# Optimization experiments

Measured on AMD Instinct MI355X. Metric: run time of the kernel, lower is better.

## Reference

```python
import jax, jax.numpy as jnp
import numpy as np

IM_H, IM_W = 240, 320
ENV_R, ENV_C = 120, 160
ENV_H, ENV_W = 8, 16
GRID = 8
NGRIDS = 6 * GRID * GRID  # 384


def _normalize(v, axis, eps=1e-6):
    return v / (jnp.linalg.norm(v, axis=axis, keepdims=True) + eps)


def setup_inputs() -> dict:
    key = jax.random.key(0)
    k1, k2, k3, k4 = jax.random.split(key, 4)
    B = 2
    normalPred = jax.random.normal(k1, (B, 3, IM_H, IM_W), dtype=jnp.float32)
    # positive depth in [0.5, 5.0] so z = -depth passes the z < -0.1 mask mostly
    depthPred = jax.random.uniform(k2, (B, IM_H, IM_W), dtype=jnp.float32, minval=0.5, maxval=5.0)
    envmapsPredImage = jax.random.uniform(k3, (B, 3, ENV_R, ENV_C, ENV_H, ENV_W), dtype=jnp.float32)
    # intrinsics must have cx = W/2, cy = H/2 (module asserts f_W_scale == f_H_scale)
    cam_K = jnp.tile(jnp.array([[300.0, 0.0, IM_W / 2.0],
                                [0.0, 300.0, IM_H / 2.0],
                                [0.0, 0.0, 1.0]], dtype=jnp.float32)[None], (B, 1, 1))
    # grid-cell centers of the 6 layout faces in LightNet coords (normally from get_grid_centers)
    verts_center_lightNet = jax.random.normal(k4, (B, 6, GRID, GRID, 3), dtype=jnp.float32) * 3.0
    return {"normalPred": normalPred, "depthPred": depthPred,
            "envmapsPredImage": envmapsPredImage, "cam_K": cam_K,
            "verts_center_lightNet": verts_center_lightNet}


def _forward(normalPred, depthPred, envmapsPredImage, cam_K, verts_center_lightNet):
    B = depthPred.shape[0]
    dt = depthPred.dtype
    # ---- back-project per-pixel 3D points from depth + intrinsics ----
    u0, v0 = IM_W / 2.0, IM_H / 2.0
    vv, uu = jnp.meshgrid(jnp.arange(IM_H, dtype=dt), jnp.arange(IM_W, dtype=dt), indexing='ij')
    f_pix = (cam_K[:, 0, 0] * (IM_W / 2.0) / cam_K[:, 0, 2]).reshape(B, 1, 1)
    z = -depthPred
    x = -(uu - u0) / f_pix * z
    y = (vv - v0) / f_pix * z
    points = jnp.stack([x, y, z], axis=1)  # [B,3,IM_H,IM_W]

    # ---- renderingLayer.forwardEnv (if_normal_only): per-pixel local frame at env res ----
    r = IM_H // ENV_R  # = IM_W // ENV_C = 2
    n = normalPred.reshape(B, 3, ENV_R, r, ENV_C, r).mean(axis=(3, 5))
    normal = _normalize(n, axis=1)                              # [B,3,eR,eC]
    up = jnp.array([0.0, 1.0, 0.0], dtype=dt).reshape(1, 3, 1, 1)
    camyProj = (up * normal).sum(axis=1, keepdims=True) * normal
    camy = _normalize(up - camyProj, axis=1)
    camx = -_normalize(jnp.cross(camy, normal, axis=1), axis=1)

    # ---- accu_light ----
    pts_s = points[:, :, ::r, ::r].transpose(0, 2, 3, 1)        # [B,eR,eC,3]
    mask = pts_s[..., 2] < -0.1                                 # [B,eR,eC]
    p_t = verts_center_lightNet.reshape(B, NGRIDS, 1, 1, 3)
    vec_to_t = p_t - pts_s[:, None]                             # [B,G,eR,eC,3]

    # A columns = [camx, camy, normal]; invert per pixel
    A = jnp.stack([camx.transpose(0, 2, 3, 1),
                   camy.transpose(0, 2, 3, 1),
                   normal.transpose(0, 2, 3, 1)], axis=-1)      # [B,eR,eC,3,3]
    A = A + 1e-6 * jnp.eye(3, dtype=dt)
    invA = jnp.linalg.inv(A)

    l_local = jnp.einsum('bhwij,bghwj->bghwi', invA, vec_to_t)  # [B,G,eR,eC,3]
    l_local = _normalize(l_local, axis=-1)
    cos_theta = l_local[..., 2]
    theta = jnp.arccos(cos_theta)
    sin_t = jnp.sin(theta) + 1e-6
    phi = jnp.arctan2(l_local[..., 1] / sin_t, l_local[..., 0] / sin_t)
    az = (phi / np.pi / 2.0 + 0.5) * ENV_W                      # [B,G,eR,eC]
    el = theta / np.pi * 2.0 * ENV_H

    # grid_sample(bilinear, padding='border', align_corners=False) on per-pixel 8x16 envmaps
    # normalized coord -> pixel coord: (uv/size*2-1 + 1)*size/2 - 0.5 = uv - 0.5
    az_f = jnp.clip(az.transpose(0, 2, 3, 1).reshape(-1, NGRIDS) - 0.5, 0.0, ENV_W - 1.0)
    el_f = jnp.clip(el.transpose(0, 2, 3, 1).reshape(-1, NGRIDS) - 0.5, 0.0, ENV_H - 1.0)
    x0 = jnp.floor(az_f); fx = az_f - x0
    y0 = jnp.floor(el_f); fy = el_f - y0
    x0i = x0.astype(jnp.int32); x1i = jnp.minimum(x0i + 1, ENV_W - 1)
    y0i = y0.astype(jnp.int32); y1i = jnp.minimum(y0i + 1, ENV_H - 1)

    env_flat = envmapsPredImage.transpose(0, 2, 3, 1, 4, 5).reshape(-1, 3, ENV_H * ENV_W)  # [Npix,3,128]

    def gather(yi, xi):
        idx = (yi * ENV_W + xi)[:, None, :]                     # [Npix,1,G]
        return jnp.take_along_axis(env_flat, idx, axis=2)       # [Npix,3,G]

    fx_ = fx[:, None, :]; fy_ = fy[:, None, :]
    val = (gather(y0i, x0i) * (1 - fx_) * (1 - fy_) +
           gather(y0i, x1i) * fx_ * (1 - fy_) +
           gather(y1i, x0i) * (1 - fx_) * fy_ +
           gather(y1i, x1i) * fx_ * fy_)                        # [Npix,3,G]

    env_acc = val.reshape(B, ENV_R, ENV_C, 3, NGRIDS).transpose(0, 3, 4, 1, 2)  # [B,3,G,eR,eC]
    mask_e = mask.astype(dt)[:, None, None]                     # [B,1,1,eR,eC]
    env_acc = env_acc * mask_e
    env_mean = (env_acc.sum((-1, -2)) / (mask_e.sum((-1, -2)) + 1e-6)).transpose(0, 2, 1)  # [B,G,3]
    return env_acc, env_mean, points, mask, vec_to_t


def reference(normalPred, depthPred, envmapsPredImage, cam_K, verts_center_lightNet):
    return _forward(normalPred, depthPred, envmapsPredImage, cam_K, verts_center_lightNet)
```

## Files before the change

### kernel.cpp

```cpp
#include <hip/hip_runtime.h>
#include <math.h>

namespace {

constexpr int IMH = 240, IMW = 320;
constexpr int ER = 120, EC = 160, EH = 8, EW = 16;
constexpr int NG = 384;
constexpr int NPIX = ER * EC;
constexpr int NB = 2;
constexpr int NTAP = EH * EW;

constexpr size_t ACC_N    = (size_t)NB * 3 * NG * NPIX;
constexpr size_t OFF_ACC  = 0;
constexpr size_t OFF_MEAN = OFF_ACC + ACC_N;
constexpr size_t MEAN_N   = (size_t)NB * NG * 3;
constexpr size_t OFF_PTS  = OFF_MEAN + MEAN_N;
constexpr size_t PTS_N    = (size_t)NB * 3 * IMH * IMW;
constexpr size_t OFF_MASK = OFF_PTS + PTS_N;
constexpr size_t MASK_N   = (size_t)NB * NPIX;
constexpr size_t OFF_VEC  = OFF_MASK + MASK_N;

constexpr int TPX   = 32;
constexpr int GLN   = 8;
constexpr int GIT   = NG / GLN;
constexpr int TILES = NPIX / TPX;
constexpr int LROW  = 3 * NTAP + 4;

constexpr size_t WS_S     = (size_t)NB * NPIX;
constexpr size_t WS_INVA  = 0;
constexpr size_t WS_PTS   = WS_INVA + 9 * WS_S;
constexpr size_t WS_PART  = WS_PTS + 3 * WS_S;
constexpr size_t PART_N   = (size_t)NB * NG * 3 * TILES;
constexpr size_t WS_CNT_HI = WS_PART + PART_N;
constexpr size_t WS_CNT_LO = WS_PART;
constexpr size_t WS_NEED_HI = (WS_CNT_HI + NB) * 4;

typedef float f32x3 __attribute__((ext_vector_type(3), aligned(4)));
typedef float f32x4 __attribute__((ext_vector_type(4)));

__device__ __forceinline__ float fpix_of(const float* K, int b) {
    return K[b * 9 + 0] * (IMW * 0.5f) / K[b * 9 + 2];
}

__device__ __forceinline__ unsigned bf16r(float f) {
    unsigned b = __float_as_uint(f);
    return (b + 0x7FFFu + ((b >> 16) & 1u)) >> 16;
}
__device__ __forceinline__ float bfload(unsigned short u) {
    return __uint_as_float((unsigned)u << 16);
}

template <int CTRL, int RMASK>
__device__ __forceinline__ float dpp_add(float s) {
    int t = __builtin_amdgcn_update_dpp(0, __float_as_int(s), CTRL, RMASK, 0xf, true);
    return s + __int_as_float(t);
}
__device__ __forceinline__ float hw_sum(float s) {
    s = dpp_add<0x111, 0xf>(s);
    s = dpp_add<0x112, 0xf>(s);
    s = dpp_add<0x114, 0xf>(s);
    s = dpp_add<0x118, 0xf>(s);
    s = dpp_add<0x142, 0xa>(s);
    return s;
}

__device__ __forceinline__ float acos_el(float x) {
    float ax = fminf(fabsf(x), 1.0f);
    float p  = fmaf(fmaf(fmaf(-0.09538315f, ax, 0.37820512f), ax, -1.08021632f),
                    ax, 7.99996873f);
    float r  = sqrtf(1.0f - ax) * p;
    return (x >= 0.0f) ? r : 16.0f - r;
}

__device__ __forceinline__ float atan2_az(float y, float x) {
    float ay = fabsf(y), ax = fabsf(x);
    float mn = fminf(ax, ay), mx = fmaxf(ax, ay);
    float a  = mn * __builtin_amdgcn_rcpf(fmaxf(mx, 1e-37f));
    float s  = a * a;
    float r  = a * fmaf(s, fmaf(s, fmaf(s, fmaf(s, 0.05305631f, -0.21677864f),
                                        0.45872349f), -0.84104627f), 2.54613763f);
    if (ay > ax) r = 4.0f - r;
    if (x < 0.0f) r = 8.0f - r;
    return fmaf(copysignf(1.0f, y), r, 8.0f);
}

__global__ void k_prep2(const float* __restrict__ normal,
                        const float* __restrict__ depth,
                        const float* __restrict__ K,
                        float* __restrict__ out,
                        float* __restrict__ ws, size_t cnt_off) {
    int t   = threadIdx.x;
    int blk = blockIdx.x;
    int idx = blk * 256 + t;
    if (blk == 0 && t < NB) ws[cnt_off + t] = 0.0f;

    {
        int b  = idx / (IMH * IMW);
        int pp = idx - b * (IMH * IMW);
        int v  = pp / IMW;
        int u  = pp - v * IMW;
        float fp = fpix_of(K, b);
        float z  = -depth[idx];
        float x  = -(((float)u - IMW * 0.5f) / fp) * z;
        float y  =  (((float)v - IMH * 0.5f) / fp) * z;
        float* P = out + OFF_PTS + (size_t)b * 3 * IMH * IMW;
        __builtin_nontemporal_store(x, P + pp);
        __builtin_nontemporal_store(y, P + pp + IMH * IMW);
        __builtin_nontemporal_store(z, P + pp + 2 * IMH * IMW);
    }

    if (blk >= (NB * NPIX) / 256) return;
    {
        int b   = idx / NPIX;
        int pix = idx - b * NPIX;
        int h   = pix / EC;
        int w   = pix - h * EC;
        int v = 2 * h, u = 2 * w;

        float fp = fpix_of(K, b);
        float z  = -depth[(size_t)b * IMH * IMW + (size_t)v * IMW + u];
        float px = -(((float)u - 160.0f) / fp) * z;
        float py =  (((float)v - 120.0f) / fp) * z;

        ws[WS_PTS + 0 * WS_S + idx] = px;
        ws[WS_PTS + 1 * WS_S + idx] = py;
        ws[WS_PTS + 2 * WS_S + idx] = z;

        float m = (z < -0.1f) ? 1.0f : 0.0f;
        __builtin_nontemporal_store(m, out + OFF_MASK + idx);
        float cm = m;
        for (int off = 32; off > 0; off >>= 1) cm += __shfl_down(cm, off);
        if ((t & 63) == 0) atomicAdd(&ws[cnt_off + b], cm);

        float n[3];
#pragma unroll
        for (int c = 0; c < 3; ++c) {
            const float* Nc = normal + ((size_t)(b * 3 + c) * IMH + v) * IMW + u;
            n[c] = 0.25f * (Nc[0] + Nc[1] + Nc[IMW] + Nc[IMW + 1]);
        }
        float nl = sqrtf(n[0]*n[0] + n[1]*n[1] + n[2]*n[2]) + 1e-6f;
        float nx = n[0] / nl, ny = n[1] / nl, nz = n[2] / nl;

        float t0 = -ny * nx, t1 = 1.0f - ny * ny, t2 = -ny * nz;
        float tl = sqrtf(t0*t0 + t1*t1 + t2*t2) + 1e-6f;
        float cy0 = t0 / tl, cy1 = t1 / tl, cy2 = t2 / tl;

        float cr0 = cy1 * nz - cy2 * ny;
        float cr1 = cy2 * nx - cy0 * nz;
        float cr2 = cy0 * ny - cy1 * nx;
        float cl = sqrtf(cr0*cr0 + cr1*cr1 + cr2*cr2) + 1e-6f;
        float cx0 = -cr0 / cl, cx1 = -cr1 / cl, cx2 = -cr2 / cl;

        float a00 = cx0 + 1e-6f, a01 = cy0,         a02 = nx;
        float a10 = cx1,         a11 = cy1 + 1e-6f, a12 = ny;
        float a20 = cx2,         a21 = cy2,         a22 = nz + 1e-6f;

        float c00 =  a11 * a22 - a12 * a21;
        float c01 = -(a10 * a22 - a12 * a20);
        float c02 =  a10 * a21 - a11 * a20;
        float det = a00 * c00 + a01 * c01 + a02 * c02;
        float id  = 1.0f / det;

        ws[WS_INVA + 0 * WS_S + idx] = c00 * id;
        ws[WS_INVA + 1 * WS_S + idx] = (a02 * a21 - a01 * a22) * id;
        ws[WS_INVA + 2 * WS_S + idx] = (a01 * a12 - a02 * a11) * id;
        ws[WS_INVA + 3 * WS_S + idx] = c01 * id;
        ws[WS_INVA + 4 * WS_S + idx] = (a00 * a22 - a02 * a20) * id;
        ws[WS_INVA + 5 * WS_S + idx] = (a02 * a10 - a00 * a12) * id;
        ws[WS_INVA + 6 * WS_S + idx] = c02 * id;
        ws[WS_INVA + 7 * WS_S + idx] = (a01 * a20 - a00 * a21) * id;
        ws[WS_INVA + 8 * WS_S + idx] = (a00 * a11 - a01 * a10) * id;
    }
}

template <bool WP>
__global__ void __launch_bounds__(256) k_env(const float* __restrict__ env,
                       const float* __restrict__ verts,
                       float* __restrict__ out,
                       float* __restrict__ ws) {
    __shared__ unsigned short lds16[TPX * LROW];

    int blk  = blockIdx.x;
    int b    = blk / TILES;
    int tile = blk - b * TILES;
    int px0  = tile * TPX;
    int t    = threadIdx.x;

    {
        const float* ebase = env + (size_t)b * 3 * NPIX * NTAP + (size_t)px0 * NTAP;
#pragma unroll
        for (int it = 0; it < 12; ++it) {
            int f   = (it * 256 + t) * 4;
            int c   = f >> 12;
            int r   = f & 4095;
            f32x4 v4 = __builtin_nontemporal_load(
                (const f32x4*)(ebase + (size_t)c * NPIX * NTAP + r));
            ushort4 u4;
            u4.x = (unsigned short)bf16r(v4.x); u4.y = (unsigned short)bf16r(v4.y);
            u4.z = (unsigned short)bf16r(v4.z); u4.w = (unsigned short)bf16r(v4.w);
            int j   = r >> 7;
            int tap = r & 127;
            *(ushort4*)(&lds16[j * LROW + c * NTAP + tap]) = u4;
        }
    }
    __syncthreads();

    int px_l  = t & 31;
    int glane = t >> 5;
    int pix   = px0 + px_l;
    int bp    = b * NPIX + pix;
    int row   = px_l * LROW;

    float px = ws[WS_PTS + 0 * WS_S + bp];
    float py = ws[WS_PTS + 1 * WS_S + bp];
    float pz = ws[WS_PTS + 2 * WS_S + bp];
    float i00 = ws[WS_INVA + 0 * WS_S + bp];
    float i01 = ws[WS_INVA + 1 * WS_S + bp];
    float i02 = ws[WS_INVA + 2 * WS_S + bp];
    float i10 = ws[WS_INVA + 3 * WS_S + bp];
    float i11 = ws[WS_INVA + 4 * WS_S + bp];
    float i12 = ws[WS_INVA + 5 * WS_S + bp];
    float i20 = ws[WS_INVA + 6 * WS_S + bp];
    float i21 = ws[WS_INVA + 7 * WS_S + bp];
    float i22 = ws[WS_INVA + 8 * WS_S + bp];
    float m = (pz < -0.1f) ? 1.0f : 0.0f;

    int g0 = glane;
    const float* vp = verts + ((size_t)b * NG + g0) * 3;
    float* pA0 = out + OFF_ACC + ((size_t)(b * 3 + 0) * NG + g0) * NPIX + pix;
    float* pA1 = out + OFF_ACC + ((size_t)(b * 3 + 1) * NG + g0) * NPIX + pix;
    float* pA2 = out + OFF_ACC + ((size_t)(b * 3 + 2) * NG + g0) * NPIX + pix;
    float* pV  = out + OFF_VEC + (((size_t)b * NG + g0) * NPIX + pix) * 3;
    float* pP  = ws + WS_PART + ((size_t)(b * NG + g0) * 3) * TILES + tile;

#pragma unroll 2
    for (int it = 0; it < GIT; ++it) {
        float vx = vp[0] - px, vy = vp[1] - py, vz = vp[2] - pz;
        f32x3 v3; v3.x = vx; v3.y = vy; v3.z = vz;
        __builtin_nontemporal_store(v3, (f32x3*)pV);

        float l0 = i00 * vx + i01 * vy + i02 * vz;
        float l1 = i10 * vx + i11 * vy + i12 * vz;
        float l2 = i20 * vx + i21 * vy + i22 * vz;
        float nl = sqrtf(l0*l0 + l1*l1 + l2*l2) + 1e-6f;
        float l2n = l2 * __builtin_amdgcn_rcpf(nl);

        float el = acos_el(l2n);
        float az = atan2_az(l1, l0);

        float azf = __builtin_amdgcn_fmed3f(az - 0.5f, 0.0f, 15.0f);
        float elf = __builtin_amdgcn_fmed3f(el - 0.5f, 0.0f, 7.0f);
        float x0 = floorf(azf), y0 = floorf(elf);
        float fx = azf - x0,    fy = elf - y0;
        int x0i = (int)x0, y0i = (int)y0;
        int x1i = min(x0i + 1, 15);
        int y1i = min(y0i + 1, 7);

        float w00 = (1.0f - fx) * (1.0f - fy);
        float w01 = fx * (1.0f - fy);
        float w10 = (1.0f - fx) * fy;
        float w11 = fx * fy;

        int a00 = row + (y0i << 4) + x0i;
        int a01 = row + (y0i << 4) + x1i;
        int a10 = row + (y1i << 4) + x0i;
        int a11 = row + (y1i << 4) + x1i;

        float v0 = (bfload(lds16[a00]) * w00 + bfload(lds16[a01]) * w01 +
                    bfload(lds16[a10]) * w10 + bfload(lds16[a11]) * w11) * m;
        float v1 = (bfload(lds16[a00 + NTAP]) * w00 + bfload(lds16[a01 + NTAP]) * w01 +
                    bfload(lds16[a10 + NTAP]) * w10 + bfload(lds16[a11 + NTAP]) * w11) * m;
        float v2 = (bfload(lds16[a00 + 2*NTAP]) * w00 + bfload(lds16[a01 + 2*NTAP]) * w01 +
                    bfload(lds16[a10 + 2*NTAP]) * w10 + bfload(lds16[a11 + 2*NTAP]) * w11) * m;

        __builtin_nontemporal_store(v0, pA0);
        __builtin_nontemporal_store(v1, pA1);
        __builtin_nontemporal_store(v2, pA2);

        if constexpr (WP) {
            float s0 = hw_sum(v0);
            float s1 = hw_sum(v1);
            float s2 = hw_sum(v2);
            if ((t & 31) == 31) {
                pP[0 * TILES] = s0;
                pP[1 * TILES] = s1;
                pP[2 * TILES] = s2;
            }
            pP += (size_t)GLN * 3 * TILES;
        }

        vp  += 3 * GLN;
        pV  += (size_t)GLN * NPIX * 3;
        pA0 += (size_t)GLN * NPIX;
        pA1 += (size_t)GLN * NPIX;
        pA2 += (size_t)GLN * NPIX;
    }
}

__global__ void k_psum(float* __restrict__ out, const float* __restrict__ ws,
                       size_t cnt_off) {
    int r = blockIdx.x;
    int l = threadIdx.x;
    const float* p = ws + WS_PART + (size_t)r * TILES;
    float s = 0.0f;
    for (int i = l; i < TILES; i += 64) s += p[i];
#pragma unroll
    for (int off = 32; off > 0; off >>= 1) s += __shfl_down(s, off);
    if (l == 0) {
        int b = r / (NG * 3);
        out[OFF_MEAN + r] = s / (ws[cnt_off + b] + 1e-6f);
    }
}

__global__ void k_mean2(float* __restrict__ out, const float* __restrict__ ws,
                        size_t cnt_off) {
    __shared__ float wsum[4];
    int blk = blockIdx.x;
    int b   = blk / (3 * NG);
    int t   = threadIdx.x;

    const float4* r4 = (const float4*)(out + OFF_ACC + (size_t)blk * NPIX);
    float s = 0.0f;
    for (int i = t; i < NPIX / 4; i += 256) {
        float4 v = r4[i];
        s += v.x + v.y + v.z + v.w;
    }
    for (int off = 32; off > 0; off >>= 1) s += __shfl_down(s, off);
    if ((t & 63) == 0) wsum[t >> 6] = s;
    __syncthreads();
    if (t == 0) {
        int rc = blk - b * 3 * NG;
        int c  = rc / NG;
        int g  = rc - c * NG;
        float tot = wsum[0] + wsum[1] + wsum[2] + wsum[3];
        out[OFF_MEAN + ((size_t)b * NG + g) * 3 + c] = tot / (ws[cnt_off + b] + 1e-6f);
    }
}

}

extern "C" void kernel_launch(void* const* d_in, const int* in_sizes, int n_in,
                              void* d_out, int out_size, void* d_ws, size_t ws_size,
                              hipStream_t stream) {
    (void)in_sizes; (void)n_in; (void)out_size;
    const float* normalPred = (const float*)d_in[0];
    const float* depthPred  = (const float*)d_in[1];
    const float* env        = (const float*)d_in[2];
    const float* K          = (const float*)d_in[3];
    const float* verts      = (const float*)d_in[4];
    float* out = (float*)d_out;
    float* ws  = (float*)d_ws;

    const bool big = ws_size >= WS_NEED_HI;
    const size_t cnt_off = big ? WS_CNT_HI : WS_CNT_LO;

    k_prep2<<<(NB * IMH * IMW) / 256, 256, 0, stream>>>(normalPred, depthPred, K, out, ws, cnt_off);
    if (big) {
        k_env<true><<<NB * TILES, 256, 0, stream>>>(env, verts, out, ws);
        k_psum<<<NB * NG * 3, 64, 0, stream>>>(out, ws, cnt_off);
    } else {
        k_env<false><<<NB * TILES, 256, 0, stream>>>(env, verts, out, ws);
        k_mean2<<<NB * 3 * NG, 256, 0, stream>>>(out, ws, cnt_off);
    }
}
```

Before: 109.3 us.

## Fuse prep kernel into env kernel, keep per-pixel frame data in LDS

Removes the separate prep kernel launch. Each env block now computes its own 32 pixels' back-projected point and inverse local frame into shared memory, and writes a slice of the full-resolution points output. The global mask count atomic is replaced by per-block partial counts that the final reduction kernels sum. This saves one launch and the workspace round trip for 12 floats per pixel, in exchange for a little extra serial prep work at the start of each env block.

New measurement: 100.8 us (median of 2 runs). -7.8%, faster.

```diff
diff --git a/kernel.cpp b/kernel.cpp
--- a/kernel.cpp
+++ b/kernel.cpp
@@ -24,16 +24,14 @@
 constexpr int GLN   = 8;
 constexpr int GIT   = NG / GLN;
 constexpr int TILES = NPIX / TPX;
+constexpr int NBLK  = NB * TILES;
 constexpr int LROW  = 3 * NTAP + 4;
 
-constexpr size_t WS_S     = (size_t)NB * NPIX;
-constexpr size_t WS_INVA  = 0;
-constexpr size_t WS_PTS   = WS_INVA + 9 * WS_S;
-constexpr size_t WS_PART  = WS_PTS + 3 * WS_S;
-constexpr size_t PART_N   = (size_t)NB * NG * 3 * TILES;
-constexpr size_t WS_CNT_HI = WS_PART + PART_N;
-constexpr size_t WS_CNT_LO = WS_PART;
-constexpr size_t WS_NEED_HI = (WS_CNT_HI + NB) * 4;
+constexpr size_t WS_PART   = 0;
+constexpr size_t PART_N    = (size_t)NB * NG * 3 * TILES;
+constexpr size_t WS_CNTP_HI = PART_N;
+constexpr size_t WS_CNTP_LO = 0;
+constexpr size_t WS_NEED_HI = (PART_N + NBLK) * 4;
 
 typedef float f32x3 __attribute__((ext_vector_type(3), aligned(4)));
 typedef float f32x4 __attribute__((ext_vector_type(4)));
@@ -84,35 +82,42 @@
     return fmaf(copysignf(1.0f, y), r, 8.0f);
 }
 
-__global__ void k_prep2(const float* __restrict__ normal,
-                        const float* __restrict__ depth,
-                        const float* __restrict__ K,
-                        float* __restrict__ out,
-                        float* __restrict__ ws, size_t cnt_off) {
-    int t   = threadIdx.x;
-    int blk = blockIdx.x;
-    int idx = blk * 256 + t;
-    if (blk == 0 && t < NB) ws[cnt_off + t] = 0.0f;
-
-    {
-        int b  = idx / (IMH * IMW);
-        int pp = idx - b * (IMH * IMW);
-        int v  = pp / IMW;
-        int u  = pp - v * IMW;
-        float fp = fpix_of(K, b);
+template <bool WP>
+__global__ void __launch_bounds__(256) k_env(const float* __restrict__ env,
+                       const float* __restrict__ verts,
+                       const float* __restrict__ normal,
+                       const float* __restrict__ depth,
+                       const float* __restrict__ K,
+                       float* __restrict__ out,
+                       float* __restrict__ ws, size_t cntp_off) {
+    __shared__ unsigned short lds16[TPX * LROW];
+    __shared__ float lprep[12 * TPX];
+
+    int blk  = blockIdx.x;
+    int b    = blk / TILES;
+    int tile = blk - b * TILES;
+    int px0  = tile * TPX;
+    int t    = threadIdx.x;
+
+
+    if (t < 128) {
+        int idx = blk * 128 + t;
+        int bb  = idx / (IMH * IMW);
+        int pp  = idx - bb * (IMH * IMW);
+        int v   = pp / IMW;
+        int u   = pp - v * IMW;
+        float fp = fpix_of(K, bb);
         float z  = -depth[idx];
         float x  = -(((float)u - IMW * 0.5f) / fp) * z;
         float y  =  (((float)v - IMH * 0.5f) / fp) * z;
-        float* P = out + OFF_PTS + (size_t)b * 3 * IMH * IMW;
+        float* P = out + OFF_PTS + (size_t)bb * 3 * IMH * IMW;
         __builtin_nontemporal_store(x, P + pp);
         __builtin_nontemporal_store(y, P + pp + IMH * IMW);
         __builtin_nontemporal_store(z, P + pp + 2 * IMH * IMW);
     }
 
-    if (blk >= (NB * NPIX) / 256) return;
-    {
-        int b   = idx / NPIX;
-        int pix = idx - b * NPIX;
+    if (t < TPX) {
+        int pix = px0 + t;
         int h   = pix / EC;
         int w   = pix - h * EC;
         int v = 2 * h, u = 2 * w;
@@ -122,15 +127,14 @@
         float px = -(((float)u - 160.0f) / fp) * z;
         float py =  (((float)v - 120.0f) / fp) * z;
 
-        ws[WS_PTS + 0 * WS_S + idx] = px;
-        ws[WS_PTS + 1 * WS_S + idx] = py;
-        ws[WS_PTS + 2 * WS_S + idx] = z;
+        lprep[0 * TPX + t] = px;
+        lprep[1 * TPX + t] = py;
+        lprep[2 * TPX + t] = z;
 
         float m = (z < -0.1f) ? 1.0f : 0.0f;
-        __builtin_nontemporal_store(m, out + OFF_MASK + idx);
-        float cm = m;
-        for (int off = 32; off > 0; off >>= 1) cm += __shfl_down(cm, off);
-        if ((t & 63) == 0) atomicAdd(&ws[cnt_off + b], cm);
+        __builtin_nontemporal_store(m, out + OFF_MASK + (size_t)b * NPIX + pix);
+        float cm = hw_sum(m);
+        if (t == 31) ws[cntp_off + blk] = cm;
 
         float n[3];
 #pragma unroll
@@ -161,30 +165,16 @@
         float det = a00 * c00 + a01 * c01 + a02 * c02;
         float id  = 1.0f / det;
 
-        ws[WS_INVA + 0 * WS_S + idx] = c00 * id;
-        ws[WS_INVA + 1 * WS_S + idx] = (a02 * a21 - a01 * a22) * id;
-        ws[WS_INVA + 2 * WS_S + idx] = (a01 * a12 - a02 * a11) * id;
-        ws[WS_INVA + 3 * WS_S + idx] = c01 * id;
-        ws[WS_INVA + 4 * WS_S + idx] = (a00 * a22 - a02 * a20) * id;
-        ws[WS_INVA + 5 * WS_S + idx] = (a02 * a10 - a00 * a12) * id;
-        ws[WS_INVA + 6 * WS_S + idx] = c02 * id;
-        ws[WS_INVA + 7 * WS_S + idx] = (a01 * a20 - a00 * a21) * id;
-        ws[WS_INVA + 8 * WS_S + idx] = (a00 * a11 - a01 * a10) * id;
-    }
-}
-
-template <bool WP>
-__global__ void __launch_bounds__(256) k_env(const float* __restrict__ env,
-                       const float* __restrict__ verts,
-                       float* __restrict__ out,
-                       float* __restrict__ ws) {
-    __shared__ unsigned short lds16[TPX * LROW];
-
-    int blk  = blockIdx.x;
-    int b    = blk / TILES;
-    int tile = blk - b * TILES;
-    int px0  = tile * TPX;
-    int t    = threadIdx.x;
+        lprep[ 3 * TPX + t] = c00 * id;
+        lprep[ 4 * TPX + t] = (a02 * a21 - a01 * a22) * id;
+        lprep[ 5 * TPX + t] = (a01 * a12 - a02 * a11) * id;
+        lprep[ 6 * TPX + t] = c01 * id;
+        lprep[ 7 * TPX + t] = (a00 * a22 - a02 * a20) * id;
+        lprep[ 8 * TPX + t] = (a02 * a10 - a00 * a12) * id;
+        lprep[ 9 * TPX + t] = c02 * id;
+        lprep[10 * TPX + t] = (a01 * a20 - a00 * a21) * id;
+        lprep[11 * TPX + t] = (a00 * a11 - a01 * a10) * id;
+    }
 
     {
         const float* ebase = env + (size_t)b * 3 * NPIX * NTAP + (size_t)px0 * NTAP;
@@ -208,21 +198,20 @@
     int px_l  = t & 31;
     int glane = t >> 5;
     int pix   = px0 + px_l;
-    int bp    = b * NPIX + pix;
     int row   = px_l * LROW;
 
-    float px = ws[WS_PTS + 0 * WS_S + bp];
-    float py = ws[WS_PTS + 1 * WS_S + bp];
-    float pz = ws[WS_PTS + 2 * WS_S + bp];
-    float i00 = ws[WS_INVA + 0 * WS_S + bp];
-    float i01 = ws[WS_INVA + 1 * WS_S + bp];
-    float i02 = ws[WS_INVA + 2 * WS_S + bp];
-    float i10 = ws[WS_INVA + 3 * WS_S + bp];
-    float i11 = ws[WS_INVA + 4 * WS_S + bp];
-    float i12 = ws[WS_INVA + 5 * WS_S + bp];
-    float i20 = ws[WS_INVA + 6 * WS_S + bp];
-    float i21 = ws[WS_INVA + 7 * WS_S + bp];
-    float i22 = ws[WS_INVA + 8 * WS_S + bp];
+    float px = lprep[0 * TPX + px_l];
+    float py = lprep[1 * TPX + px_l];
+    float pz = lprep[2 * TPX + px_l];
+    float i00 = lprep[ 3 * TPX + px_l];
+    float i01 = lprep[ 4 * TPX + px_l];
+    float i02 = lprep[ 5 * TPX + px_l];
+    float i10 = lprep[ 6 * TPX + px_l];
+    float i11 = lprep[ 7 * TPX + px_l];
+    float i12 = lprep[ 8 * TPX + px_l];
+    float i20 = lprep[ 9 * TPX + px_l];
+    float i21 = lprep[10 * TPX + px_l];
+    float i22 = lprep[11 * TPX + px_l];
     float m = (pz < -0.1f) ? 1.0f : 0.0f;
 
     int g0 = glane;
@@ -298,23 +287,25 @@
 }
 
 __global__ void k_psum(float* __restrict__ out, const float* __restrict__ ws,
-                       size_t cnt_off) {
+                       size_t cntp_off) {
     int r = blockIdx.x;
     int l = threadIdx.x;
-    const float* p = ws + WS_PART + (size_t)r * TILES;
-    float s = 0.0f;
-    for (int i = l; i < TILES; i += 64) s += p[i];
+    int b = r / (NG * 3);
+    const float* p  = ws + WS_PART + (size_t)r * TILES;
+    const float* cp = ws + cntp_off + (size_t)b * TILES;
+    float s = 0.0f, c = 0.0f;
+    for (int i = l; i < TILES; i += 64) { s += p[i]; c += cp[i]; }
 #pragma unroll
-    for (int off = 32; off > 0; off >>= 1) s += __shfl_down(s, off);
-    if (l == 0) {
-        int b = r / (NG * 3);
-        out[OFF_MEAN + r] = s / (ws[cnt_off + b] + 1e-6f);
-    }
+    for (int off = 32; off > 0; off >>= 1) {
+        s += __shfl_down(s, off);
+        c += __shfl_down(c, off);
+    }
+    if (l == 0) out[OFF_MEAN + r] = s / (c + 1e-6f);
 }
 
 __global__ void k_mean2(float* __restrict__ out, const float* __restrict__ ws,
-                        size_t cnt_off) {
-    __shared__ float wsum[4];
+                        size_t cntp_off) {
+    __shared__ float wsum[8];
     int blk = blockIdx.x;
     int b   = blk / (3 * NG);
     int t   = threadIdx.x;
@@ -325,15 +316,22 @@
         float4 v = r4[i];
         s += v.x + v.y + v.z + v.w;
     }
-    for (int off = 32; off > 0; off >>= 1) s += __shfl_down(s, off);
-    if ((t & 63) == 0) wsum[t >> 6] = s;
+    const float* cp = ws + cntp_off + (size_t)b * TILES;
+    float c = 0.0f;
+    for (int i = t; i < TILES; i += 256) c += cp[i];
+    for (int off = 32; off > 0; off >>= 1) {
+        s += __shfl_down(s, off);
+        c += __shfl_down(c, off);
+    }
+    if ((t & 63) == 0) { wsum[t >> 6] = s; wsum[4 + (t >> 6)] = c; }
     __syncthreads();
     if (t == 0) {
         int rc = blk - b * 3 * NG;
-        int c  = rc / NG;
-        int g  = rc - c * NG;
+        int ch = rc / NG;
+        int g  = rc - ch * NG;
         float tot = wsum[0] + wsum[1] + wsum[2] + wsum[3];
-        out[OFF_MEAN + ((size_t)b * NG + g) * 3 + c] = tot / (ws[cnt_off + b] + 1e-6f);
+        float cnt = wsum[4] + wsum[5] + wsum[6] + wsum[7];
+        out[OFF_MEAN + ((size_t)b * NG + g) * 3 + ch] = tot / (cnt + 1e-6f);
     }
 }
 
@@ -352,14 +350,13 @@
     float* ws  = (float*)d_ws;
 
     const bool big = ws_size >= WS_NEED_HI;
-    const size_t cnt_off = big ? WS_CNT_HI : WS_CNT_LO;
-
-    k_prep2<<<(NB * IMH * IMW) / 256, 256, 0, stream>>>(normalPred, depthPred, K, out, ws, cnt_off);
+    const size_t cntp_off = big ? WS_CNTP_HI : WS_CNTP_LO;
+
     if (big) {
-        k_env<true><<<NB * TILES, 256, 0, stream>>>(env, verts, out, ws);
-        k_psum<<<NB * NG * 3, 64, 0, stream>>>(out, ws, cnt_off);
+        k_env<true><<<NBLK, 256, 0, stream>>>(env, verts, normalPred, depthPred, K, out, ws, cntp_off);
+        k_psum<<<NB * NG * 3, 64, 0, stream>>>(out, ws, cntp_off);
     } else {
-        k_env<false><<<NB * TILES, 256, 0, stream>>>(env, verts, out, ws);
-        k_mean2<<<NB * 3 * NG, 256, 0, stream>>>(out, ws, cnt_off);
-    }
-}
+        k_env<false><<<NBLK, 256, 0, stream>>>(env, verts, normalPred, depthPred, K, out, ws, cntp_off);
+        k_mean2<<<NB * 3 * NG, 256, 0, stream>>>(out, ws, cntp_off);
+    }
+}
```
